# Kernel tuning notes

Measured on AMD Instinct MI355X. Metric: run time of the kernel, lower is better.

The kernel has to match this reference:

```python
import jax, jax.numpy as jnp
import numpy as np

D_MODEL = 1024
NUM_HEADS = 16
HEAD_DIM = D_MODEL // NUM_HEADS
B, S = 4, 2048


def setup_inputs() -> dict:
    key = jax.random.key(0)
    ks = jax.random.split(key, 11)
    scale = 1.0 / np.sqrt(D_MODEL)
    inp = {
        "query": jax.random.normal(ks[0], (B, S, D_MODEL), dtype=jnp.float32),
        "key": jax.random.normal(ks[1], (B, S, D_MODEL), dtype=jnp.float32),
        "value": jax.random.normal(ks[2], (B, S, D_MODEL), dtype=jnp.float32),
        "Wq": jax.random.normal(ks[3], (D_MODEL, D_MODEL), dtype=jnp.float32) * scale,
        "bq": jnp.zeros((D_MODEL,), dtype=jnp.float32),
        "Wk": jax.random.normal(ks[4], (D_MODEL, D_MODEL), dtype=jnp.float32) * scale,
        "bk": jnp.zeros((D_MODEL,), dtype=jnp.float32),
        "Wv": jax.random.normal(ks[5], (D_MODEL, D_MODEL), dtype=jnp.float32) * scale,
        "bv": jnp.zeros((D_MODEL,), dtype=jnp.float32),
        "Wo": jax.random.normal(ks[6], (D_MODEL, D_MODEL), dtype=jnp.float32) * scale,
        "bo": jnpp.zeros((D_MODEL,), dtype=jnp.float32) if False else jnp.zeros((D_MODEL,), dtype=jnp.float32),
    }
    return inp


def reference(query, key, value, Wq, bq, Wk, bk, Wv, bv, Wo, bo):
    # Linear projections (torch Linear: x @ W.T + b), split into heads: [B,H,S,Dh]
    def split_heads(x):
        b, s, _ = x.shape
        return x.reshape(b, s, NUM_HEADS, HEAD_DIM).transpose(0, 2, 1, 3)

    q = split_heads(query @ Wq.T + bq)
    k = split_heads(key @ Wk.T + bk)
    v = split_heads(value @ Wv.T + bv)

    # Explicit attention: [B,H,S,S] scores, softmax, AV
    scores = jnp.einsum("bhqd,bhkd->bhqk", q, k) / np.sqrt(HEAD_DIM).astype(np.float32)
    attn = jax.nn.softmax(scores, axis=-1)
    ctx = jnp.einsum("bhqk,bhkd->bhqd", attn, v)

    # Merge heads and output projection
    b = ctx.shape[0]
    ctx = ctx.transpose(0, 2, 1, 3).reshape(b, -1, D_MODEL)
    return ctx @ Wo.T + bo
```

## Files before the change

kernel.cpp:

```cpp
#include <hip/hip_runtime.h>
#include <stdint.h>

#define DMODEL 1024
#define NHEADS 16
#define HDIM   64
#define BB     4
#define SS     2048
#define MM     (BB*SS)
#define QKV_ELEMS ((size_t)8388608)

typedef unsigned short ushort_t;
typedef __bf16    bf16x8 __attribute__((ext_vector_type(8)));
typedef _Float16  half4  __attribute__((ext_vector_type(4)));
typedef float     floatx4 __attribute__((ext_vector_type(4)));

__device__ inline ushort_t f32_to_bf16(float f) {
    union { float f; uint32_t u; } v; v.f = f;
    uint32_t r = v.u + 0x7FFF + ((v.u >> 16) & 1);
    return (ushort_t)(r >> 16);
}
__device__ inline ushort_t f32_to_f16u(float f) {
    union { _Float16 h; ushort_t u; } v; v.h = (_Float16)f; return v.u;
}
__device__ inline void glds16(const void* g, void* l) {
    __builtin_amdgcn_global_load_lds(
        (const __attribute__((address_space(1))) unsigned int*)g,
        (__attribute__((address_space(3))) unsigned int*)l, 16, 0, 0);
}

__global__ __launch_bounds__(256) void convert_bf16(const float* __restrict__ in,
                                                    ushort_t* __restrict__ out) {
    size_t i = ((size_t)blockIdx.x * 256 + threadIdx.x) * 8;
    float4 a = *(const float4*)&in[i];
    float4 b = *(const float4*)&in[i + 4];
    ushort_t t[8];
    t[0] = f32_to_bf16(a.x); t[1] = f32_to_bf16(a.y);
    t[2] = f32_to_bf16(a.z); t[3] = f32_to_bf16(a.w);
    t[4] = f32_to_bf16(b.x); t[5] = f32_to_bf16(b.y);
    t[6] = f32_to_bf16(b.z); t[7] = f32_to_bf16(b.w);
    *(uint4*)&out[i] = *(uint4*)t;
}

__global__ __launch_bounds__(256) void convert_w3(
    const float* __restrict__ w0, const float* __restrict__ w1, const float* __restrict__ w2,
    ushort_t* __restrict__ o0, ushort_t* __restrict__ o1, ushort_t* __restrict__ o2) {
    const float* src = (blockIdx.y == 0) ? w0 : (blockIdx.y == 1) ? w1 : w2;
    ushort_t*    dst = (blockIdx.y == 0) ? o0 : (blockIdx.y == 1) ? o1 : o2;
    size_t i = ((size_t)blockIdx.x * 256 + threadIdx.x) * 8;
    float4 a = *(const float4*)&src[i];
    float4 b = *(const float4*)&src[i + 4];
    ushort_t t[8];
    t[0] = f32_to_bf16(a.x); t[1] = f32_to_bf16(a.y);
    t[2] = f32_to_bf16(a.z); t[3] = f32_to_bf16(a.w);
    t[4] = f32_to_bf16(b.x); t[5] = f32_to_bf16(b.y);
    t[6] = f32_to_bf16(b.z); t[7] = f32_to_bf16(b.w);
    *(uint4*)&dst[i] = *(uint4*)t;
}

template<int OUT>
__global__ __launch_bounds__(256) void gemm_bf16(
    const ushort_t* __restrict__ A, const ushort_t* __restrict__ W,
    const float* __restrict__ bias, void* __restrict__ O, float scale)
{
    __shared__ ushort_t As[128 * 32];
    __shared__ ushort_t Bs[128 * 32];

    const int tid  = threadIdx.x;
    const int lane = tid & 63;
    const int quad = lane >> 4;
    const int l15  = lane & 15;
    const int wid  = tid >> 6;
    const int wr   = wid >> 1, wc = wid & 1;
    const int m0   = blockIdx.y * 128;
    const int n0   = blockIdx.x * 128;

    floatx4 acc[4][4];
    #pragma unroll
    for (int i = 0; i < 4; i++)
        #pragma unroll
        for (int j = 0; j < 4; j++)
            acc[i][j] = (floatx4){0.f, 0.f, 0.f, 0.f};

    for (int k0 = 0; k0 < DMODEL; k0 += 32) {
        #pragma unroll
        for (int j = 0; j < 2; j++) {
            const int p   = tid + j * 256;
            const int row = p >> 2, cc = p & 3;
            glds16(&A[(size_t)(m0 + row) * DMODEL + k0 + cc * 8], &As[p * 8]);
            glds16(&W[(size_t)(n0 + row) * DMODEL + k0 + cc * 8], &Bs[p * 8]);
        }
        __syncthreads();

        bf16x8 af[4], bf[4];
        #pragma unroll
        for (int i = 0; i < 4; i++)
            af[i] = *(const bf16x8*)&As[(wr * 64 + i * 16 + l15) * 32 + quad * 8];
        #pragma unroll
        for (int j = 0; j < 4; j++)
            bf[j] = *(const bf16x8*)&Bs[(wc * 64 + j * 16 + l15) * 32 + quad * 8];
        #pragma unroll
        for (int i = 0; i < 4; i++)
            #pragma unroll
            for (int j = 0; j < 4; j++)
                acc[i][j] = __builtin_amdgcn_mfma_f32_16x16x32_bf16(af[i], bf[j], acc[i][j], 0, 0, 0);
        __syncthreads();
    }

    #pragma unroll
    for (int j = 0; j < 4; j++) {
        const int n = n0 + wc * 64 + j * 16 + l15;
        const float bn = bias[n];
        #pragma unroll
        for (int i = 0; i < 4; i++) {
            #pragma unroll
            for (int r = 0; r < 4; r++) {
                const int m = m0 + wr * 64 + i * 16 + quad * 4 + r;
                float v = (acc[i][j][r] + bn) * scale;
                if (OUT == 0) {
                    const int b = m >> 11, s = m & 2047;
                    const int h = n >> 6,  dh = n & 63;
                    ((ushort_t*)O)[(((size_t)(b * NHEADS + h)) * SS + s) * HDIM + dh] = f32_to_bf16(v);
                } else if (OUT == 1) {
                    const int b = m >> 11, s = m & 2047;
                    const int h = n >> 6,  dh = n & 63;
                    ((ushort_t*)O)[(((size_t)(b * NHEADS + h)) * SS + s) * HDIM + dh] = f32_to_f16u(v);
                } else {
                    ((float*)O)[(size_t)m * DMODEL + n] = v;
                }
            }
        }
    }
}

__global__ __launch_bounds__(256) void attn_kernel(
    const ushort_t* __restrict__ Q, const ushort_t* __restrict__ K,
    const ushort_t* __restrict__ V, ushort_t* __restrict__ ctx)
{
    constexpr int LDV = 72;
    __shared__ ushort_t smem[9216];
    ushort_t* Ks = smem;
    ushort_t* Vt = smem + 4096;
    ushort_t* Tr = smem;

    const int tid  = threadIdx.x;
    const int lane = tid & 63;
    const int wid  = tid >> 6;
    const int quad = lane >> 4;
    const int l15  = lane & 15;
    const int bh   = blockIdx.y;
    const int b    = bh >> 4, h = bh & 15;
    const int q0   = blockIdx.x * 128 + wid * 32;

    const ushort_t* Qb = Q + (size_t)bh * SS * HDIM;
    const ushort_t* Kb = K + (size_t)bh * SS * HDIM;
    const ushort_t* Vb = V + (size_t)bh * SS * HDIM;

    bf16x8 qf[2][2];
    #pragma unroll
    for (int qt = 0; qt < 2; qt++)
        #pragma unroll
        for (int c = 0; c < 2; c++)
            qf[qt][c] = *(const bf16x8*)&Qb[(size_t)(q0 + qt * 16 + l15) * HDIM + c * 32 + quad * 8];

    floatx4 acc[2][4];
    #pragma unroll
    for (int qt = 0; qt < 2; qt++)
        #pragma unroll
        for (int dt = 0; dt < 4; dt++)
            acc[qt][dt] = (floatx4){0.f, 0.f, 0.f, 0.f};
    float mrun[2] = {-1e30f, -1e30f};
    float lrun[2] = {0.f, 0.f};

    const int kp = tid & 31;
    const int dc = tid >> 5;

    for (int kt = 0; kt < SS; kt += 64) {
        #pragma unroll
        for (int j = 0; j < 2; j++) {
            const int p   = tid + j * 256;
            const int row = p >> 3;
            const int cc  = (p & 7) ^ (row & 7);
            glds16(&Kb[(size_t)(kt + row) * HDIM + cc * 8], &Ks[p * 8]);
        }
        {
            ushort_t ua[8], ub[8];
            *(uint4*)ua = *(const uint4*)&Vb[(size_t)(kt + 2 * kp) * HDIM + dc * 8];
            *(uint4*)ub = *(const uint4*)&Vb[(size_t)(kt + 2 * kp + 1) * HDIM + dc * 8];
            #pragma unroll
            for (int i = 0; i < 8; i++)
                *(uint32_t*)&Vt[(dc * 8 + i) * LDV + 2 * kp] = (uint32_t)ua[i] | ((uint32_t)ub[i] << 16);
        }
        __syncthreads();

        bf16x8 kf[4][2];
        #pragma unroll
        for (int nt = 0; nt < 4; nt++) {
            const int row = nt * 16 + l15;
            #pragma unroll
            for (int c = 0; c < 2; c++) {
                const int pos = (c * 4 + quad) ^ (row & 7);
                kf[nt][c] = *(const bf16x8*)&Ks[row * 64 + pos * 8];
            }
        }
        half4 vf[4][4];
        #pragma unroll
        for (int kb = 0; kb < 4; kb++)
            #pragma unroll
            for (int dt = 0; dt < 4; dt++)
                vf[kb][dt] = *(const half4*)&Vt[(dt * 16 + l15) * LDV + kb * 16 + quad * 4];

        #pragma unroll
        for (int qt = 0; qt < 2; qt++) {
            floatx4 s[4];
            #pragma unroll
            for (int nt = 0; nt < 4; nt++) {
                floatx4 cz = (floatx4){0.f, 0.f, 0.f, 0.f};
                cz = __builtin_amdgcn_mfma_f32_16x16x32_bf16(kf[nt][0], qf[qt][0], cz, 0, 0, 0);
                cz = __builtin_amdgcn_mfma_f32_16x16x32_bf16(kf[nt][1], qf[qt][1], cz, 0, 0, 0);
                s[nt] = cz;
            }
            float mx = s[0][0];
            #pragma unroll
            for (int nt = 0; nt < 4; nt++)
                #pragma unroll
                for (int r = 0; r < 4; r++) mx = fmaxf(mx, s[nt][r]);
            mx = fmaxf(mx, __shfl_xor(mx, 16));
            mx = fmaxf(mx, __shfl_xor(mx, 32));
            const float mnew  = fmaxf(mrun[qt], mx);
            const float alpha = __expf(mrun[qt] - mnew);
            mrun[qt] = mnew;

            float ps = 0.f;
            half4 pf[4];
            #pragma unroll
            for (int nt = 0; nt < 4; nt++) {
                #pragma unroll
                for (int r = 0; r < 4; r++) {
                    const float p = __expf(s[nt][r] - mnew);
                    ps += p;
                    pf[nt][r] = (_Float16)p;
                }
            }
            ps += __shfl_xor(ps, 16);
            ps += __shfl_xor(ps, 32);
            lrun[qt] = lrun[qt] * alpha + ps;

            #pragma unroll
            for (int dt = 0; dt < 4; dt++) acc[qt][dt] *= alpha;
            #pragma unroll
            for (int kb = 0; kb < 4; kb++)
                #pragma unroll
                for (int dt = 0; dt < 4; dt++)
                    acc[qt][dt] = __builtin_amdgcn_mfma_f32_16x16x16f16(vf[kb][dt], pf[kb], acc[qt][dt], 0, 0, 0);
        }
        __syncthreads();
    }

    const float inv0 = 1.f / lrun[0], inv1 = 1.f / lrun[1];
    ushort_t* Tw = Tr + wid * (32 * LDV);
    #pragma unroll
    for (int qt = 0; qt < 2; qt++) {
        const float inv = qt ? inv1 : inv0;
        #pragma unroll
        for (int dt = 0; dt < 4; dt++)
            #pragma unroll
            for (int r = 0; r < 4; r++)
                Tw[(qt * 16 + l15) * LDV + dt * 16 + quad * 4 + r] = f32_to_bf16(acc[qt][dt][r] * inv);
    }
    const int row = lane >> 1, hf = lane & 1;
    const ushort_t* src = Tw + row * LDV + hf * 32;
    ushort_t* dst = ctx + ((size_t)(b * SS) + q0 + row) * DMODEL + h * HDIM + hf * 32;
    #pragma unroll
    for (int i = 0; i < 4; i++)
        *(uint4*)(dst + i * 8) = *(const uint4*)(src + i * 8);
}

extern "C" void kernel_launch(void* const* d_in, const int* in_sizes, int n_in,
                              void* d_out, int out_size, void* d_ws, size_t ws_size,
                              hipStream_t stream) {
    (void)in_sizes; (void)n_in; (void)out_size; (void)ws_size;
    const float* query = (const float*)d_in[0];
    const float* key_  = (const float*)d_in[1];
    const float* value = (const float*)d_in[2];
    const float* Wq = (const float*)d_in[3];
    const float* bq = (const float*)d_in[4];
    const float* Wk = (const float*)d_in[5];
    const float* bk = (const float*)d_in[6];
    const float* Wv = (const float*)d_in[7];
    const float* bv = (const float*)d_in[8];
    const float* Wo = (const float*)d_in[9];
    const float* bo = (const float*)d_in[10];
    float* out = (float*)d_out;

    ushort_t* tmp = (ushort_t*)d_ws;
    ushort_t* Qw  = tmp + QKV_ELEMS;
    ushort_t* Kw  = Qw + QKV_ELEMS;
    ushort_t* Vw  = Kw + QKV_ELEMS;
    ushort_t* ctx = tmp;
    ushort_t* Wqb = (ushort_t*)d_out;
    ushort_t* Wkb = Wqb + 1048576;
    ushort_t* Wvb = Wkb + 1048576;
    ushort_t* Wob = Qw;

    dim3 blk(256);
    dim3 gg(DMODEL / 128, MM / 128);

    hipLaunchKernelGGL(convert_w3, dim3(512, 3), blk, 0, stream, Wq, Wk, Wv, Wqb, Wkb, Wvb);

    hipLaunchKernelGGL(convert_bf16, dim3(4096), blk, 0, stream, query, tmp);
    hipLaunchKernelGGL((gemm_bf16<0>), gg, blk, 0, stream, tmp, Wqb, bq, (void*)Qw, 0.125f);
    hipLaunchKernelGGL(convert_bf16, dim3(4096), blk, 0, stream, key_, tmp);
    hipLaunchKernelGGL((gemm_bf16<0>), gg, blk, 0, stream, tmp, Wkb, bk, (void*)Kw, 1.0f);
    hipLaunchKernelGGL(convert_bf16, dim3(4096), blk, 0, stream, value, tmp);
    hipLaunchKernelGGL((gemm_bf16<1>), gg, blk, 0, stream, tmp, Wvb, bv, (void*)Vw, 1.0f);

    hipLaunchKernelGGL(attn_kernel, dim3(SS / 128, BB * NHEADS), blk, 0, stream, Qw, Kw, Vw, ctx);

    hipLaunchKernelGGL(convert_bf16, dim3(512), blk, 0, stream, Wo, Wob);
    hipLaunchKernelGGL((gemm_bf16<2>), gg, blk, 0, stream, ctx, Wob, bo, (void*)out, 1.0f);
}
```

Before: 433.8 us.

## Double-buffer GEMM and attention tiles, use exp2 softmax with packed f16 sums

The GEMM k-loop now double-buffers its LDS tiles. The next tile's loads are issued before computing on the current one, and one barrier per iteration is removed. The attention kernel double-buffers its K and transposed-V tiles and remaps blocks over a 1D grid so that heads interleave. Softmax folds log2(e) into the Q scale and uses exp2, packs probabilities with cvt_pkrtz, and sums them with fdot2. The extra LDS reduces occupancy headroom, and summing in f16 with round-toward-zero changes precision slightly.

Measured after the change: 404.8 us. -6.7%, faster.

```diff
diff --git a/kernel.cpp b/kernel.cpp
--- a/kernel.cpp
+++ b/kernel.cpp
@@ -10,8 +10,9 @@
 #define QKV_ELEMS ((size_t)8388608)
 
 typedef unsigned short ushort_t;
-typedef __bf16    bf16x8 __attribute__((ext_vector_type(8)));
-typedef _Float16  half4  __attribute__((ext_vector_type(4)));
+typedef __bf16    bf16x8  __attribute__((ext_vector_type(8)));
+typedef _Float16  half4   __attribute__((ext_vector_type(4)));
+typedef _Float16  half2_t __attribute__((ext_vector_type(2)));
 typedef float     floatx4 __attribute__((ext_vector_type(4)));
 
 __device__ inline ushort_t f32_to_bf16(float f) {
@@ -21,6 +22,9 @@
 }
 __device__ inline ushort_t f32_to_f16u(float f) {
     union { _Float16 h; ushort_t u; } v; v.h = (_Float16)f; return v.u;
+}
+__device__ inline half2_t pkrtz(float a, float b) {
+    return __builtin_bit_cast(half2_t, __builtin_amdgcn_cvt_pkrtz(a, b));
 }
 __device__ inline void glds16(const void* g, void* l) {
     __builtin_amdgcn_global_load_lds(
@@ -62,8 +66,8 @@
     const ushort_t* __restrict__ A, const ushort_t* __restrict__ W,
     const float* __restrict__ bias, void* __restrict__ O, float scale)
 {
-    __shared__ ushort_t As[128 * 32];
-    __shared__ ushort_t Bs[128 * 32];
+    __shared__ ushort_t As[2 * 128 * 32];
+    __shared__ ushort_t Bs[2 * 128 * 32];
 
     const int tid  = threadIdx.x;
     const int lane = tid & 63;
@@ -81,29 +85,36 @@
         for (int j = 0; j < 4; j++)
             acc[i][j] = (floatx4){0.f, 0.f, 0.f, 0.f};
 
+    #pragma unroll
+    for (int j = 0; j < 2; j++) {
+        const int p = tid + j * 256, row = p >> 2, cc = p & 3;
+        glds16(&A[(size_t)(m0 + row) * DMODEL + cc * 8], &As[p * 8]);
+        glds16(&W[(size_t)(n0 + row) * DMODEL + cc * 8], &Bs[p * 8]);
+    }
+
     for (int k0 = 0; k0 < DMODEL; k0 += 32) {
+        const int cb = ((k0 >> 5) & 1) * (128 * 32);
+        const int nbo = (128 * 32) - cb;
+        __syncthreads();
+        const int kn = (k0 + 32) & (DMODEL - 1);
         #pragma unroll
         for (int j = 0; j < 2; j++) {
-            const int p   = tid + j * 256;
-            const int row = p >> 2, cc = p & 3;
-            glds16(&A[(size_t)(m0 + row) * DMODEL + k0 + cc * 8], &As[p * 8]);
-            glds16(&W[(size_t)(n0 + row) * DMODEL + k0 + cc * 8], &Bs[p * 8]);
-        }
-        __syncthreads();
-
+            const int p = tid + j * 256, row = p >> 2, cc = p & 3;
+            glds16(&A[(size_t)(m0 + row) * DMODEL + kn + cc * 8], &As[nbo + p * 8]);
+            glds16(&W[(size_t)(n0 + row) * DMODEL + kn + cc * 8], &Bs[nbo + p * 8]);
+        }
         bf16x8 af[4], bf[4];
         #pragma unroll
         for (int i = 0; i < 4; i++)
-            af[i] = *(const bf16x8*)&As[(wr * 64 + i * 16 + l15) * 32 + quad * 8];
+            af[i] = *(const bf16x8*)&As[cb + (wr * 64 + i * 16 + l15) * 32 + quad * 8];
         #pragma unroll
         for (int j = 0; j < 4; j++)
-            bf[j] = *(const bf16x8*)&Bs[(wc * 64 + j * 16 + l15) * 32 + quad * 8];
+            bf[j] = *(const bf16x8*)&Bs[cb + (wc * 64 + j * 16 + l15) * 32 + quad * 8];
         #pragma unroll
         for (int i = 0; i < 4; i++)
             #pragma unroll
             for (int j = 0; j < 4; j++)
                 acc[i][j] = __builtin_amdgcn_mfma_f32_16x16x32_bf16(af[i], bf[j], acc[i][j], 0, 0, 0);
-        __syncthreads();
     }
 
     #pragma unroll
@@ -118,12 +129,12 @@
                 float v = (acc[i][j][r] + bn) * scale;
                 if (OUT == 0) {
                     const int b = m >> 11, s = m & 2047;
-                    const int h = n >> 6,  dh = n & 63;
-                    ((ushort_t*)O)[(((size_t)(b * NHEADS + h)) * SS + s) * HDIM + dh] = f32_to_bf16(v);
+                    const int hh = n >> 6, dh = n & 63;
+                    ((ushort_t*)O)[(((size_t)(b * NHEADS + hh)) * SS + s) * HDIM + dh] = f32_to_bf16(v);
                 } else if (OUT == 1) {
                     const int b = m >> 11, s = m & 2047;
-                    const int h = n >> 6,  dh = n & 63;
-                    ((ushort_t*)O)[(((size_t)(b * NHEADS + h)) * SS + s) * HDIM + dh] = f32_to_f16u(v);
+                    const int hh = n >> 6, dh = n & 63;
+                    ((ushort_t*)O)[(((size_t)(b * NHEADS + hh)) * SS + s) * HDIM + dh] = f32_to_f16u(v);
                 } else {
                     ((float*)O)[(size_t)m * DMODEL + n] = v;
                 }
@@ -132,14 +143,13 @@
     }
 }
 
-__global__ __launch_bounds__(256) void attn_kernel(
+__global__ __launch_bounds__(256, 4) void attn_kernel(
     const ushort_t* __restrict__ Q, const ushort_t* __restrict__ K,
     const ushort_t* __restrict__ V, ushort_t* __restrict__ ctx)
 {
     constexpr int LDV = 72;
-    __shared__ ushort_t smem[9216];
-    ushort_t* Ks = smem;
-    ushort_t* Vt = smem + 4096;
+    constexpr int VOFF = 2 * 4096;
+    __shared__ ushort_t smem[2 * 4096 + 2 * 64 * LDV];
     ushort_t* Tr = smem;
 
     const int tid  = threadIdx.x;
@@ -147,9 +157,10 @@
     const int wid  = tid >> 6;
     const int quad = lane >> 4;
     const int l15  = lane & 15;
-    const int bh   = blockIdx.y;
+    const int bid  = blockIdx.x;
+    const int bh   = (bid & 7) * 8 + (bid >> 7);
     const int b    = bh >> 4, h = bh & 15;
-    const int q0   = blockIdx.x * 128 + wid * 32;
+    const int q0   = ((bid >> 3) & 15) * 128 + wid * 32;
 
     const ushort_t* Qb = Q + (size_t)bh * SS * HDIM;
     const ushort_t* Kb = K + (size_t)bh * SS * HDIM;
@@ -174,23 +185,39 @@
     const int kp = tid & 31;
     const int dc = tid >> 5;
 
+    #pragma unroll
+    for (int j = 0; j < 2; j++) {
+        const int p = tid + j * 256, row = p >> 3, cc = (p & 7) ^ (row & 7);
+        glds16(&Kb[(size_t)row * HDIM + cc * 8], &smem[p * 8]);
+    }
+    {
+        ushort_t ua[8], ub[8];
+        *(uint4*)ua = *(const uint4*)&Vb[(size_t)(2 * kp) * HDIM + dc * 8];
+        *(uint4*)ub = *(const uint4*)&Vb[(size_t)(2 * kp + 1) * HDIM + dc * 8];
+        #pragma unroll
+        for (int i = 0; i < 8; i++)
+            *(uint32_t*)&smem[VOFF + (dc * 8 + i) * LDV + 2 * kp] = (uint32_t)ua[i] | ((uint32_t)ub[i] << 16);
+    }
+
+    const half2_t one2 = {(_Float16)1.f, (_Float16)1.f};
+
     for (int kt = 0; kt < SS; kt += 64) {
+        const int cur = ((kt >> 6) & 1);
+        const int ko  = cur * 4096;
+        const int kon = 4096 - ko;
+        const int vo  = VOFF + cur * (64 * LDV);
+        const int von = VOFF + (64 * LDV) - cur * (64 * LDV);
+        __syncthreads();
+
+        const int ktn = (kt + 64) & (SS - 1);
         #pragma unroll
         for (int j = 0; j < 2; j++) {
-            const int p   = tid + j * 256;
-            const int row = p >> 3;
-            const int cc  = (p & 7) ^ (row & 7);
-            glds16(&Kb[(size_t)(kt + row) * HDIM + cc * 8], &Ks[p * 8]);
-        }
-        {
-            ushort_t ua[8], ub[8];
-            *(uint4*)ua = *(const uint4*)&Vb[(size_t)(kt + 2 * kp) * HDIM + dc * 8];
-            *(uint4*)ub = *(const uint4*)&Vb[(size_t)(kt + 2 * kp + 1) * HDIM + dc * 8];
-            #pragma unroll
-            for (int i = 0; i < 8; i++)
-                *(uint32_t*)&Vt[(dc * 8 + i) * LDV + 2 * kp] = (uint32_t)ua[i] | ((uint32_t)ub[i] << 16);
-        }
-        __syncthreads();
+            const int p = tid + j * 256, row = p >> 3, cc = (p & 7) ^ (row & 7);
+            glds16(&Kb[(size_t)(ktn + row) * HDIM + cc * 8], &smem[kon + p * 8]);
+        }
+        ushort_t ua[8], ub[8];
+        *(uint4*)ua = *(const uint4*)&Vb[(size_t)(ktn + 2 * kp) * HDIM + dc * 8];
+        *(uint4*)ub = *(const uint4*)&Vb[(size_t)(ktn + 2 * kp + 1) * HDIM + dc * 8];
 
         bf16x8 kf[4][2];
         #pragma unroll
@@ -199,7 +226,7 @@
             #pragma unroll
             for (int c = 0; c < 2; c++) {
                 const int pos = (c * 4 + quad) ^ (row & 7);
-                kf[nt][c] = *(const bf16x8*)&Ks[row * 64 + pos * 8];
+                kf[nt][c] = *(const bf16x8*)&smem[ko + row * 64 + pos * 8];
             }
         }
         half4 vf[4][4];
@@ -207,7 +234,7 @@
         for (int kb = 0; kb < 4; kb++)
             #pragma unroll
             for (int dt = 0; dt < 4; dt++)
-                vf[kb][dt] = *(const half4*)&Vt[(dt * 16 + l15) * LDV + kb * 16 + quad * 4];
+                vf[kb][dt] = *(const half4*)&smem[vo + (dt * 16 + l15) * LDV + kb * 16 + quad * 4];
 
         #pragma unroll
         for (int qt = 0; qt < 2; qt++) {
@@ -227,19 +254,24 @@
             mx = fmaxf(mx, __shfl_xor(mx, 16));
             mx = fmaxf(mx, __shfl_xor(mx, 32));
             const float mnew  = fmaxf(mrun[qt], mx);
-            const float alpha = __expf(mrun[qt] - mnew);
+            const float alpha = __builtin_amdgcn_exp2f(mrun[qt] - mnew);
             mrun[qt] = mnew;
 
             float ps = 0.f;
             half4 pf[4];
             #pragma unroll
             for (int nt = 0; nt < 4; nt++) {
-                #pragma unroll
-                for (int r = 0; r < 4; r++) {
-                    const float p = __expf(s[nt][r] - mnew);
-                    ps += p;
-                    pf[nt][r] = (_Float16)p;
-                }
+                const float p0 = __builtin_amdgcn_exp2f(s[nt][0] - mnew);
+                const float p1 = __builtin_amdgcn_exp2f(s[nt][1] - mnew);
+                const float p2 = __builtin_amdgcn_exp2f(s[nt][2] - mnew);
+                const float p3 = __builtin_amdgcn_exp2f(s[nt][3] - mnew);
+                const half2_t ha = pkrtz(p0, p1);
+                const half2_t hb = pkrtz(p2, p3);
+                ps = __builtin_amdgcn_fdot2(ha, one2, ps, false);
+                ps = __builtin_amdgcn_fdot2(hb, one2, ps, false);
+                union { half4 h4; half2_t h2[2]; } u;
+                u.h2[0] = ha; u.h2[1] = hb;
+                pf[nt] = u.h4;
             }
             ps += __shfl_xor(ps, 16);
             ps += __shfl_xor(ps, 32);
@@ -253,9 +285,13 @@
                 for (int dt = 0; dt < 4; dt++)
                     acc[qt][dt] = __builtin_amdgcn_mfma_f32_16x16x16f16(vf[kb][dt], pf[kb], acc[qt][dt], 0, 0, 0);
         }
-        __syncthreads();
-    }
-
+
+        #pragma unroll
+        for (int i = 0; i < 8; i++)
+            *(uint32_t*)&smem[von + (dc * 8 + i) * LDV + 2 * kp] = (uint32_t)ua[i] | ((uint32_t)ub[i] << 16);
+    }
+
+    __syncthreads();
     const float inv0 = 1.f / lrun[0], inv1 = 1.f / lrun[1];
     ushort_t* Tw = Tr + wid * (32 * LDV);
     #pragma unroll
@@ -308,13 +344,13 @@
     hipLaunchKernelGGL(convert_w3, dim3(512, 3), blk, 0, stream, Wq, Wk, Wv, Wqb, Wkb, Wvb);
 
     hipLaunchKernelGGL(convert_bf16, dim3(4096), blk, 0, stream, query, tmp);
-    hipLaunchKernelGGL((gemm_bf16<0>), gg, blk, 0, stream, tmp, Wqb, bq, (void*)Qw, 0.125f);
+    hipLaunchKernelGGL((gemm_bf16<0>), gg, blk, 0, stream, tmp, Wqb, bq, (void*)Qw, 0.18033688011f);
     hipLaunchKernelGGL(convert_bf16, dim3(4096), blk, 0, stream, key_, tmp);
     hipLaunchKernelGGL((gemm_bf16<0>), gg, blk, 0, stream, tmp, Wkb, bk, (void*)Kw, 1.0f);
     hipLaunchKernelGGL(convert_bf16, dim3(4096), blk, 0, stream, value, tmp);
     hipLaunchKernelGGL((gemm_bf16<1>), gg, blk, 0, stream, tmp, Wvb, bv, (void*)Vw, 1.0f);
 
-    hipLaunchKernelGGL(attn_kernel, dim3(SS / 128, BB * NHEADS), blk, 0, stream, Qw, Kw, Vw, ctx);
+    hipLaunchKernelGGL(attn_kernel, dim3(1024), blk, 0, stream, Qw, Kw, Vw, ctx);
 
     hipLaunchKernelGGL(convert_bf16, dim3(512), blk, 0, stream, Wo, Wob);
     hipLaunchKernelGGL((gemm_bf16<2>), gg, blk, 0, stream, ctx, Wob, bo, (void*)out, 1.0f);
```
